# Kernel optimization log

Hardware: AMD Instinct MI355X
Metric: run time of the kernel (lower is better)

Reference implementation:

```python
import jax, jax.numpy as jnp
import numpy as np

INPUT_SIZE = 968
HIDDEN = 128
ESP = 1e-6


def _gru_scan(xp, w_hh, b_hh):
    # xp: [T, B, 3H] precomputed input projections; returns [T, B, H]
    B = xp.shape[1]
    h0 = jnp.zeros((B, HIDDEN), dtype=xp.dtype)

    def step(h, xp_t):
        gi_r, gi_z, gi_n = jnp.split(xp_t, 3, axis=-1)
        gh = h @ w_hh.T + b_hh
        gh_r, gh_z, gh_n = jnp.split(gh, 3, axis=-1)
        r = jax.nn.sigmoid(gi_r + gh_r)
        z = jax.nn.sigmoid(gi_z + gh_z)
        n = jnp.tanh(gi_n + r * gh_n)
        h_new = (1.0 - z) * n + z * h
        return h_new, h_new

    _, hs = jax.lax.scan(step, h0, xp)
    return hs


def _bigru_ln(x, w_ih_f, w_hh_f, b_ih_f, b_hh_f,
              w_ih_b, w_hh_b, b_ih_b, b_hh_b, ln_w, ln_b):
    # x: [B, T, D] (batch_first)
    # precompute input projections as one big GEMM per direction
    xp_f = jnp.einsum('btd,gd->btg', x, w_ih_f) + b_ih_f  # [B,T,3H]
    xp_b = jnp.einsum('btd,gd->btg', x, w_ih_b) + b_ih_b
    xp_f = jnp.swapaxes(xp_f, 0, 1)  # [T,B,3H]
    xp_b = jnp.swapaxes(xp_b, 0, 1)[::-1]  # reversed time for backward dir

    h_f = _gru_scan(xp_f, w_hh_f, b_hh_f)          # [T,B,H]
    h_b = _gru_scan(xp_b, w_hh_b, b_hh_b)[::-1]    # [T,B,H], un-reverse

    out = jnp.concatenate([h_f, h_b], axis=-1)     # [T,B,2H]
    out = jnp.swapaxes(out, 0, 1)                  # [B,T,2H]

    # LayerNormal: uses unbiased std (torch.std default, ddof=1), clamped
    mu = jnp.mean(out, axis=-1, keepdims=True)
    sigma = jnp.std(out, axis=-1, keepdims=True, ddof=1)
    sigma = jnp.maximum(sigma, ESP)
    return (out - mu) / sigma * ln_w + ln_b


def setup_inputs() -> dict:
    key = jax.random.key(0)
    ks = jax.random.split(key, 10)
    B, T = 64, 512
    s_ih = 1.0 / np.sqrt(HIDDEN)
    u = lambda k, shape: jax.random.uniform(k, shape, jnp.float32, -s_ih, s_ih)
    return {
        'x': jax.random.normal(ks[0], (B, T, INPUT_SIZE), jnp.float32),
        'w_ih_f': u(ks[1], (3 * HIDDEN, INPUT_SIZE)),
        'w_hh_f': u(ks[2], (3 * HIDDEN, HIDDEN)),
        'b_ih_f': u(ks[3], (3 * HIDDEN,)),
        'b_hh_f': u(ks[4], (3 * HIDDEN,)),
        'w_ih_b': u(ks[5], (3 * HIDDEN, INPUT_SIZE)),
        'w_hh_b': u(ks[6], (3 * HIDDEN, HIDDEN)),
        'b_ih_b': u(ks[7], (3 * HIDDEN,)),
        'b_hh_b': u(ks[8], (3 * HIDDEN,)),
        'ln_w': jnp.ones((2 * HIDDEN,), jnp.float32),
        'ln_b': jnp.zeros((2 * HIDDEN,), jnp.float32),
    }


def reference(x, w_ih_f, w_hh_f, b_ih_f, b_hh_f,
              w_ih_b, w_hh_b, b_ih_b, b_hh_b, ln_w, ln_b):
    return _bigru_ln(x, w_ih_f, w_hh_f, b_ih_f, b_hh_f,
                     w_ih_b, w_hh_b, b_ih_b, b_hh_b, ln_w, ln_b)
```

## Files before the change

### kernel.cpp

```cpp
#include <hip/hip_runtime.h>
#include <stdint.h>


#define LOG2E 1.4426950408889634f
#define TT 512
#define D_IN 968
#define KP 992
#define NOUT 768
#define HID 128

typedef __attribute__((ext_vector_type(8))) short short8;
typedef __attribute__((ext_vector_type(4))) float f32x4;
typedef __attribute__((ext_vector_type(4))) unsigned int u32x4;
typedef __attribute__((ext_vector_type(2))) unsigned int u32x2;

__device__ __forceinline__ unsigned short f2bf(float f) {
  unsigned u = __builtin_bit_cast(unsigned, f);
  u += 0x7FFFu + ((u >> 16) & 1u);
  return (unsigned short)(u >> 16);
}
__device__ __forceinline__ unsigned pack2bf(float a, float b) {
  return (unsigned)f2bf(a) | ((unsigned)f2bf(b) << 16);
}
__device__ __forceinline__ float exp2_(float x) { return __builtin_amdgcn_exp2f(x); }
__device__ __forceinline__ float rcp_(float x)  { return __builtin_amdgcn_rcpf(x); }

__device__ __forceinline__ void async_load16(const void* g, void* l) {
  __builtin_amdgcn_global_load_lds(
      (const __attribute__((address_space(1))) unsigned int*)g,
      (__attribute__((address_space(3))) unsigned int*)l, 16, 0, 0);
}

__device__ __forceinline__ void wg_barrier_lds() {
  asm volatile("s_waitcnt lgkmcnt(0)\n\ts_barrier" ::: "memory");
}

#define WIH_BYTES (NOUT * KP * 2)
#define WHH_BYTES (NOUT * HID * 2)
#define BIAS_BYTES 3072
#define BASE_OFF (WIH_BYTES + WHH_BYTES + BIAS_BYTES)
#define XBF_BYTES ((size_t)32768 * KP * 2)
#define XP_BYTES ((size_t)32768 * NOUT * 4)

__global__ __launch_bounds__(256) void kx_convert(const float* __restrict__ X,
                                                  unsigned short* __restrict__ Xb) {
  const long row = blockIdx.x;
  const int t = threadIdx.x;
  if (t < 242) {
    f32x4 v = *(const f32x4*)(X + row * D_IN + t * 4);
    u32x2 p = {pack2bf(v.x, v.y), pack2bf(v.z, v.w)};
    *(u32x2*)(Xb + row * KP + t * 4) = p;
  } else if (t < 248) {
    *(u32x2*)(Xb + row * KP + t * 4) = (u32x2){0, 0};
  }
}

__global__ __launch_bounds__(256) void k0_convert(
    const float* __restrict__ wihf, const float* __restrict__ whhf,
    const float* __restrict__ bihf, const float* __restrict__ wihb,
    const float* __restrict__ whhb, const float* __restrict__ bihb,
    unsigned short* __restrict__ wih16, unsigned short* __restrict__ whh16,
    float* __restrict__ bias_s) {
  int blk = blockIdx.x, tid = threadIdx.x;
  if (blk < NOUT) {
    int n = blk;
    float sc = ((n % 384) < 256) ? LOG2E : 2.0f * LOG2E;
    const float* src = (n < 384) ? (wihf + (long)n * D_IN) : (wihb + (long)(n - 384) * D_IN);
    for (int c = 0; c < 4; c++) {
      int k = c * 256 + tid;
      if (k < KP) {
        float v = (k < D_IN) ? src[k] * sc : 0.0f;
        wih16[(long)n * KP + k] = f2bf(v);
      }
    }
  } else if (blk < NOUT + 96) {
    int e0 = ((blk - NOUT) * 256 + tid) * 4;
    for (int i = 0; i < 4; i++) {
      int e = e0 + i;
      int m = e >> 7, k = e & 127;
      float sc = ((m % 384) < 256) ? LOG2E : 2.0f * LOG2E;
      float v = (m < 384) ? whhf[m * HID + k] : whhb[(m - 384) * HID + k];
      whh16[e] = f2bf(v * sc);
    }
  } else {
    for (int c = 0; c < 3; c++) {
      int n = c * 256 + tid;
      if (n < NOUT) {
        float sc = ((n % 384) < 256) ? LOG2E : 2.0f * LOG2E;
        bias_s[n] = ((n < 384) ? bihf[n] : bihb[n - 384]) * sc;
      }
    }
  }
}

__global__ __launch_bounds__(256, 2) void k1_gemm_fast(
    const unsigned short* __restrict__ Xb, const unsigned short* __restrict__ W,
    const float* __restrict__ bias_s, float* __restrict__ XP) {
  __shared__ unsigned short As[128 * 32];
  __shared__ unsigned short Bs[128 * 32];

  const int tid = threadIdx.x;
  const int lane = tid & 63, w = tid >> 6;
  const int q = lane >> 4, l15 = lane & 15;
  const int wr = w >> 1, wc = w & 1;
  const int nt = blockIdx.x;
  const int mt = blockIdx.y;
  const long R0 = (long)mt * 128;
  const int C0 = nt * 128;

  f32x4 acc[4][4];
#pragma unroll
  for (int i = 0; i < 4; i++)
#pragma unroll
    for (int j = 0; j < 4; j++) acc[i][j] = {0.f, 0.f, 0.f, 0.f};

  for (int it = 0; it < 31; it++) {
    const int k0 = it * 32;
#pragma unroll
    for (int c = 0; c < 2; c++) {
      int idx = c * 256 + w * 64 + lane;
      int row = idx >> 2, koff = (idx & 3) * 8;
      async_load16(Xb + (R0 + row) * KP + k0 + koff,
                   ((char*)As) + (c * 256 + w * 64) * 16);
      async_load16(W + (long)(C0 + row) * KP + k0 + koff,
                   ((char*)Bs) + (c * 256 + w * 64) * 16);
    }
    __syncthreads();
    short8 af[4], bf[4];
#pragma unroll
    for (int i = 0; i < 4; i++)
      af[i] = *(const short8*)&As[(wr * 64 + i * 16 + l15) * 32 + q * 8];
#pragma unroll
    for (int j = 0; j < 4; j++)
      bf[j] = *(const short8*)&Bs[(wc * 64 + j * 16 + l15) * 32 + q * 8];
#pragma unroll
    for (int i = 0; i < 4; i++)
#pragma unroll
      for (int j = 0; j < 4; j++)
        acc[i][j] = __builtin_amdgcn_mfma_f32_16x16x32_bf16(af[i], bf[j], acc[i][j], 0, 0, 0);
    __syncthreads();
  }
  float bv[4];
#pragma unroll
  for (int j = 0; j < 4; j++) bv[j] = bias_s[C0 + wc * 64 + j * 16 + l15];
#pragma unroll
  for (int i = 0; i < 4; i++)
#pragma unroll
    for (int j = 0; j < 4; j++) {
      int col = C0 + wc * 64 + j * 16 + l15;
      long Rb = R0 + wr * 64 + i * 16 + q * 4;
#pragma unroll
      for (int r = 0; r < 4; r++)
        XP[(Rb + r) * NOUT + col] = acc[i][j][r] + bv[j];
    }
}

#define AS_STRIDE 40
__global__ __launch_bounds__(256, 2) void k1_gemm_slow(
    const float* __restrict__ X, const unsigned short* __restrict__ W,
    const float* __restrict__ bias_s, float* __restrict__ XP) {
  __shared__ unsigned short As[128 * AS_STRIDE];
  __shared__ unsigned short Bs[128 * 32];
  const int tid = threadIdx.x;
  const int lane = tid & 63, w = tid >> 6;
  const int q = lane >> 4, l15 = lane & 15;
  const int wr = w >> 1, wc = w & 1;
  const int nt = blockIdx.x, mt = blockIdx.y;
  const long R0 = (long)mt * 128;
  const int C0 = nt * 128;
  const int ar = tid >> 1, ahf = tid & 1;
  f32x4 acc[4][4];
#pragma unroll
  for (int i = 0; i < 4; i++)
#pragma unroll
    for (int j = 0; j < 4; j++) acc[i][j] = {0.f, 0.f, 0.f, 0.f};
  const float* arow = X + (R0 + ar) * D_IN;
  for (int it = 0; it < 31; it++) {
    int k0 = it * 32;
    unsigned pk[8];
#pragma unroll
    for (int c = 0; c < 4; c++) {
      int kc = k0 + ahf * 16 + c * 4;
      kc = (kc <= 964) ? kc : 964;
      f32x4 v = *(const f32x4*)(arow + kc);
      pk[c * 2 + 0] = pack2bf(v.x, v.y);
      pk[c * 2 + 1] = pack2bf(v.z, v.w);
    }
    unsigned short* adst = &As[ar * AS_STRIDE + ahf * 16];
    *(u32x4*)adst = (u32x4){pk[0], pk[1], pk[2], pk[3]};
    *(u32x4*)(adst + 8) = (u32x4){pk[4], pk[5], pk[6], pk[7]};
#pragma unroll
    for (int c = 0; c < 2; c++) {
      int idx = c * 256 + w * 64 + lane;
      int brow = idx >> 2, koff = (idx & 3) * 8;
      async_load16(W + (long)(C0 + brow) * KP + k0 + koff,
                   ((char*)Bs) + (c * 256 + w * 64) * 16);
    }
    __syncthreads();
    short8 af[4], bf[4];
#pragma unroll
    for (int i = 0; i < 4; i++)
      af[i] = *(const short8*)&As[(wr * 64 + i * 16 + l15) * AS_STRIDE + q * 8];
#pragma unroll
    for (int j = 0; j < 4; j++)
      bf[j] = *(const short8*)&Bs[(wc * 64 + j * 16 + l15) * 32 + q * 8];
#pragma unroll
    for (int i = 0; i < 4; i++)
#pragma unroll
      for (int j = 0; j < 4; j++)
        acc[i][j] = __builtin_amdgcn_mfma_f32_16x16x32_bf16(af[i], bf[j], acc[i][j], 0, 0, 0);
    __syncthreads();
  }
  float bv[4];
#pragma unroll
  for (int j = 0; j < 4; j++) bv[j] = bias_s[C0 + wc * 64 + j * 16 + l15];
#pragma unroll
  for (int i = 0; i < 4; i++)
#pragma unroll
    for (int j = 0; j < 4; j++) {
      int col = C0 + wc * 64 + j * 16 + l15;
      long Rb = R0 + wr * 64 + i * 16 + q * 4;
#pragma unroll
      for (int r = 0; r < 4; r++)
        XP[(Rb + r) * NOUT + col] = acc[i][j][r] + bv[j];
    }
}

#define PF 4

__global__ __launch_bounds__(512) void k2_gru(
    const unsigned short* __restrict__ WHH, const float* __restrict__ XP,
    const float* __restrict__ bhh_f, const float* __restrict__ bhh_b,
    float* __restrict__ OUT) {
  __shared__ unsigned short Hl[2][16 * 128];

  const int tid = threadIdx.x;
  const int lane = tid & 63, w = tid >> 6;
  const int q = lane >> 4, b = lane & 15;
  const int dir = blockIdx.x & 1, bg = blockIdx.x >> 1;
  const int j0 = w * 16 + q * 4;

  for (int i = tid; i < 2 * 16 * 128; i += 512) ((unsigned short*)Hl)[i] = 0;

  short8 afr[3][4];
#pragma unroll
  for (int g = 0; g < 3; g++)
#pragma unroll
    for (int kt = 0; kt < 4; kt++) {
      int row = dir * 384 + g * 128 + w * 16 + b;
      afr[g][kt] = *(const short8*)(WHH + (long)row * HID + kt * 32 + q * 8);
    }
  const float* bhh = dir ? bhh_b : bhh_f;
  f32x4 bh[3];
#pragma unroll
  for (int g = 0; g < 3; g++) {
    f32x4 t = *(const f32x4*)(bhh + g * 128 + j0);
    bh[g] = t * ((g < 2) ? LOG2E : 2.0f * LOG2E);
  }

  const long gi_base = (long)(bg * 16 + b) * TT * NOUT + dir * 384 + j0;
  const long out_base = (long)(bg * 16 + b) * TT * 256 + dir * 128 + j0;

  f32x4 gR[PF], gZ[PF], gN[PF];
#pragma unroll
  for (int u = 0; u < PF; u++) {
    const int td = dir ? (TT - 1 - u) : u;
    const float* gb = XP + gi_base + (long)td * NOUT;
    gR[u] = *(const f32x4*)(gb);
    gZ[u] = *(const f32x4*)(gb + 128);
    gN[u] = *(const f32x4*)(gb + 256);
  }
  f32x4 h = {0.f, 0.f, 0.f, 0.f};
  __syncthreads();

  for (int t0 = 0; t0 < TT; t0 += PF) {
#pragma unroll
    for (int u = 0; u < PF; u++) {
      const int t = t0 + u;
      const int cur = t & 1, nxt = cur ^ 1;
      const int td = dir ? (TT - 1 - t) : t;

      short8 bfr[4];
#pragma unroll
      for (int kt = 0; kt < 4; kt++) {
        int ch = ((kt * 4 + q) ^ (b & 7)) * 8;
        bfr[kt] = *(const short8*)&Hl[cur][b * 128 + ch];
      }
      f32x4 accR = {0.f, 0.f, 0.f, 0.f};
      f32x4 accZ = {0.f, 0.f, 0.f, 0.f};
      f32x4 accN = {0.f, 0.f, 0.f, 0.f};
#pragma unroll
      for (int kt = 0; kt < 4; kt++) {
        accR = __builtin_amdgcn_mfma_f32_16x16x32_bf16(afr[0][kt], bfr[kt], accR, 0, 0, 0);
        accZ = __builtin_amdgcn_mfma_f32_16x16x32_bf16(afr[1][kt], bfr[kt], accZ, 0, 0, 0);
        accN = __builtin_amdgcn_mfma_f32_16x16x32_bf16(afr[2][kt], bfr[kt], accN, 0, 0, 0);
      }
      f32x4 hnew;
#pragma unroll
      for (int i = 0; i < 4; i++) {
        float pr = gR[u][i] + accR[i] + bh[0][i];
        float pz = gZ[u][i] + accZ[i] + bh[1][i];
        float r = rcp_(1.0f + exp2_(-pr));
        float z = rcp_(1.0f + exp2_(-pz));
        float pn = gN[u][i] + r * (accN[i] + bh[2][i]);
        float n = 1.0f - 2.0f * rcp_(exp2_(pn) + 1.0f);
        hnew[i] = n + z * (h[i] - n);
      }
      h = hnew;
      {
        int tn = t + PF;
        tn = (tn < TT) ? tn : (TT - 1);
        const int tdn = dir ? (TT - 1 - tn) : tn;
        const float* gb = XP + gi_base + (long)tdn * NOUT;
        gR[u] = *(const f32x4*)(gb);
        gZ[u] = *(const f32x4*)(gb + 128);
        gN[u] = *(const f32x4*)(gb + 256);
      }
      {
        int ch = ((j0 >> 3) ^ (b & 7)) * 8 + (j0 & 7);
        u32x2 hv = {pack2bf(hnew[0], hnew[1]), pack2bf(hnew[2], hnew[3])};
        *(u32x2*)&Hl[nxt][b * 128 + ch] = hv;
      }
      *(f32x4*)(OUT + out_base + (long)td * 256) = hnew;
      wg_barrier_lds();
    }
  }
}

__global__ __launch_bounds__(256) void k3_ln(float* __restrict__ OUT,
                                             const float* __restrict__ lnw,
                                             const float* __restrict__ lnb) {
  const int tid = threadIdx.x, lane = tid & 63, w = tid >> 6;
  const long row = (long)blockIdx.x * 4 + w;
  float* p = OUT + row * 256 + lane * 4;
  f32x4 x = *(const f32x4*)p;
  float s = x[0] + x[1] + x[2] + x[3];
  float s2 = x[0] * x[0] + x[1] * x[1] + x[2] * x[2] + x[3] * x[3];
#pragma unroll
  for (int m = 1; m < 64; m <<= 1) {
    s += __shfl_xor(s, m, 64);
    s2 += __shfl_xor(s2, m, 64);
  }
  float mu = s * (1.0f / 256.0f);
  float var = (s2 - s * mu) * (1.0f / 255.0f);
  var = fmaxf(var, 0.0f);
  float sig = fmaxf(sqrtf(var), 1e-6f);
  float inv = 1.0f / sig;
  f32x4 wv = *(const f32x4*)(lnw + lane * 4);
  f32x4 bv = *(const f32x4*)(lnb + lane * 4);
  f32x4 y;
#pragma unroll
  for (int i = 0; i < 4; i++) y[i] = (x[i] - mu) * inv * wv[i] + bv[i];
  *(f32x4*)p = y;
}

extern "C" void kernel_launch(void* const* d_in, const int* in_sizes, int n_in,
                              void* d_out, int out_size, void* d_ws, size_t ws_size,
                              hipStream_t stream) {
  const float* x = (const float*)d_in[0];
  const float* wihf = (const float*)d_in[1];
  const float* whhf = (const float*)d_in[2];
  const float* bihf = (const float*)d_in[3];
  const float* bhhf = (const float*)d_in[4];
  const float* wihb = (const float*)d_in[5];
  const float* whhb = (const float*)d_in[6];
  const float* bihb = (const float*)d_in[7];
  const float* bhhb = (const float*)d_in[8];
  const float* lnw = (const float*)d_in[9];
  const float* lnb = (const float*)d_in[10];

  char* ws = (char*)d_ws;
  unsigned short* wih16 = (unsigned short*)ws;
  unsigned short* whh16 = (unsigned short*)(ws + WIH_BYTES);
  float* bias_s = (float*)(ws + WIH_BYTES + WHH_BYTES);
  float* out = (float*)d_out;

  const size_t need_fast = (size_t)BASE_OFF + XBF_BYTES + XP_BYTES;

  hipLaunchKernelGGL(k0_convert, dim3(768 + 96 + 1), dim3(256), 0, stream,
                     wihf, whhf, bihf, wihb, whhb, bihb, wih16, whh16, bias_s);

  float* xp;
  if (ws_size >= need_fast) {
    unsigned short* xbf = (unsigned short*)(ws + BASE_OFF);
    xp = (float*)(ws + BASE_OFF + XBF_BYTES);
    hipLaunchKernelGGL(kx_convert, dim3(32768), dim3(256), 0, stream, x, xbf);
    hipLaunchKernelGGL(k1_gemm_fast, dim3(6, 256), dim3(256), 0, stream,
                       xbf, wih16, bias_s, xp);
  } else {
    xp = (float*)(ws + BASE_OFF);
    hipLaunchKernelGGL(k1_gemm_slow, dim3(6, 256), dim3(256), 0, stream,
                       x, wih16, bias_s, xp);
  }
  hipLaunchKernelGGL(k2_gru, dim3(8), dim3(512), 0, stream, whh16, xp, bhhf, bhhb, out);
  hipLaunchKernelGGL(k3_ln, dim3(8192), dim3(256), 0, stream, out, lnw, lnb);
}
```

Baseline: 683.2 us.

## Restructure GRU recurrence step: split MFMA chains, fold hidden biases, pointer-increment prefetch

Folds the r and z hidden-state biases into the precomputed input-projection bias so the recurrent step does fewer adds per element. The serial GRU step now splits each gate's 4-deep dependent MFMA chain into two independent 2-deep chains that are summed afterwards, shortening the critical latency per timestep. Address arithmetic is replaced by incremented pointers, and the tail iterations no longer issue redundant prefetch loads. The gate math is vectorized so the transcendental instructions can be grouped. The cost is a few extra vector adds per step and more registers held live.

Measured after the change: 703.3 us. 1.03x slower.

```diff
diff --git a/kernel.cpp b/kernel.cpp
--- a/kernel.cpp
+++ b/kernel.cpp
@@ -59,6 +59,7 @@
     const float* __restrict__ wihf, const float* __restrict__ whhf,
     const float* __restrict__ bihf, const float* __restrict__ wihb,
     const float* __restrict__ whhb, const float* __restrict__ bihb,
+    const float* __restrict__ bhhf, const float* __restrict__ bhhb,
     unsigned short* __restrict__ wih16, unsigned short* __restrict__ whh16,
     float* __restrict__ bias_s) {
   int blk = blockIdx.x, tid = threadIdx.x;
@@ -86,8 +87,12 @@
     for (int c = 0; c < 3; c++) {
       int n = c * 256 + tid;
       if (n < NOUT) {
-        float sc = ((n % 384) < 256) ? LOG2E : 2.0f * LOG2E;
-        bias_s[n] = ((n < 384) ? bihf[n] : bihb[n - 384]) * sc;
+        int g = (n % 384) >> 7;
+        float sc = (g < 2) ? LOG2E : 2.0f * LOG2E;
+        float bi = (n < 384) ? bihf[n] : bihb[n - 384];
+        float bh = (n < 384) ? bhhf[n] : bhhb[n - 384];
+        float v = (g < 2) ? (bi + bh) : bi;
+        bias_s[n] = v * sc;
       }
     }
   }
@@ -226,7 +231,72 @@
     }
 }
 
+__device__ __forceinline__ f32x4 gru_gate(f32x4 accR, f32x4 accZ, f32x4 accN,
+                                          f32x4 gr, f32x4 gz, f32x4 gn,
+                                          f32x4 bh2, f32x4 h) {
+  f32x4 pr = gr + accR;
+  f32x4 pz = gz + accZ;
+  f32x4 er, ez;
+#pragma unroll
+  for (int i = 0; i < 4; i++) er[i] = exp2_(-pr[i]);
+#pragma unroll
+  for (int i = 0; i < 4; i++) ez[i] = exp2_(-pz[i]);
+  f32x4 dr = er + 1.0f, dz = ez + 1.0f;
+  f32x4 r, z;
+#pragma unroll
+  for (int i = 0; i < 4; i++) r[i] = rcp_(dr[i]);
+#pragma unroll
+  for (int i = 0; i < 4; i++) z[i] = rcp_(dz[i]);
+  f32x4 pn = gn + r * (accN + bh2);
+  f32x4 en;
+#pragma unroll
+  for (int i = 0; i < 4; i++) en[i] = exp2_(pn[i]);
+  f32x4 dn = en + 1.0f, invn;
+#pragma unroll
+  for (int i = 0; i < 4; i++) invn[i] = rcp_(dn[i]);
+  f32x4 n = 1.0f - 2.0f * invn;
+  return n + z * (h - n);
+}
+
 #define PF 4
+#define MFMA_BF16 __builtin_amdgcn_mfma_f32_16x16x32_bf16
+
+#define K2_STEP(U, REFILL)                                                    \
+  {                                                                           \
+    const unsigned short* hb = ((U) & 1) ? hrd1 : hrd0;                       \
+    short8 b0 = *(const short8*)(hb + ch0);                                   \
+    short8 b1 = *(const short8*)(hb + ch1);                                   \
+    short8 b2 = *(const short8*)(hb + ch2);                                   \
+    short8 b3 = *(const short8*)(hb + ch3);                                   \
+    f32x4 cgR = gRr[U], cgZ = gZr[U], cgN = gNr[U];                           \
+    if (REFILL) {                                                             \
+      gRr[U] = *(const f32x4*)(gp);                                           \
+      gZr[U] = *(const f32x4*)(gp + 128);                                     \
+      gNr[U] = *(const f32x4*)(gp + 256);                                     \
+      gp += gstep;                                                            \
+    }                                                                         \
+    const f32x4 zz = {0.f, 0.f, 0.f, 0.f};                                    \
+    f32x4 aR0 = MFMA_BF16(afr[0][0], b0, zz, 0, 0, 0);                        \
+    f32x4 aZ0 = MFMA_BF16(afr[1][0], b0, zz, 0, 0, 0);                        \
+    f32x4 aN0 = MFMA_BF16(afr[2][0], b0, zz, 0, 0, 0);                        \
+    f32x4 aR1 = MFMA_BF16(afr[0][2], b2, zz, 0, 0, 0);                        \
+    f32x4 aZ1 = MFMA_BF16(afr[1][2], b2, zz, 0, 0, 0);                        \
+    f32x4 aN1 = MFMA_BF16(afr[2][2], b2, zz, 0, 0, 0);                        \
+    aR0 = MFMA_BF16(afr[0][1], b1, aR0, 0, 0, 0);                             \
+    aZ0 = MFMA_BF16(afr[1][1], b1, aZ0, 0, 0, 0);                             \
+    aN0 = MFMA_BF16(afr[2][1], b1, aN0, 0, 0, 0);                             \
+    aR1 = MFMA_BF16(afr[0][3], b3, aR1, 0, 0, 0);                             \
+    aZ1 = MFMA_BF16(afr[1][3], b3, aZ1, 0, 0, 0);                             \
+    aN1 = MFMA_BF16(afr[2][3], b3, aN1, 0, 0, 0);                             \
+    f32x4 hnew = gru_gate(aR0 + aR1, aZ0 + aZ1, aN0 + aN1,                    \
+                          cgR, cgZ, cgN, bh2, h);                             \
+    h = hnew;                                                                 \
+    u32x2 hv = {pack2bf(hnew[0], hnew[1]), pack2bf(hnew[2], hnew[3])};        \
+    *(u32x2*)(((U) & 1) ? hwr0 : hwr1) = hv;                                  \
+    *(f32x4*)op = hnew;                                                       \
+    op += ostep;                                                              \
+    wg_barrier_lds();                                                         \
+  }
 
 __global__ __launch_bounds__(512) void k2_gru(
     const unsigned short* __restrict__ WHH, const float* __restrict__ XP,
@@ -251,80 +321,46 @@
       afr[g][kt] = *(const short8*)(WHH + (long)row * HID + kt * 32 + q * 8);
     }
   const float* bhh = dir ? bhh_b : bhh_f;
-  f32x4 bh[3];
-#pragma unroll
-  for (int g = 0; g < 3; g++) {
-    f32x4 t = *(const f32x4*)(bhh + g * 128 + j0);
-    bh[g] = t * ((g < 2) ? LOG2E : 2.0f * LOG2E);
-  }
-
-  const long gi_base = (long)(bg * 16 + b) * TT * NOUT + dir * 384 + j0;
-  const long out_base = (long)(bg * 16 + b) * TT * 256 + dir * 128 + j0;
-
-  f32x4 gR[PF], gZ[PF], gN[PF];
+  f32x4 bh2 = (*(const f32x4*)(bhh + 256 + j0)) * (2.0f * LOG2E);
+
+  const long gstep = dir ? -(long)NOUT : (long)NOUT;
+  const long ostep = dir ? -256L : 256L;
+  const int td0 = dir ? (TT - 1) : 0;
+  const float* gp = XP + ((long)(bg * 16 + b) * TT + td0) * NOUT + dir * 384 + j0;
+  float* op = OUT + ((long)(bg * 16 + b) * TT + td0) * 256 + dir * 128 + j0;
+
+  f32x4 gRr[PF], gZr[PF], gNr[PF];
 #pragma unroll
   for (int u = 0; u < PF; u++) {
-    const int td = dir ? (TT - 1 - u) : u;
-    const float* gb = XP + gi_base + (long)td * NOUT;
-    gR[u] = *(const f32x4*)(gb);
-    gZ[u] = *(const f32x4*)(gb + 128);
-    gN[u] = *(const f32x4*)(gb + 256);
-  }
+    gRr[u] = *(const f32x4*)(gp);
+    gZr[u] = *(const f32x4*)(gp + 128);
+    gNr[u] = *(const f32x4*)(gp + 256);
+    gp += gstep;
+  }
+
+  const int ch0 = ((0 * 4 + q) ^ (b & 7)) * 8;
+  const int ch1 = ((1 * 4 + q) ^ (b & 7)) * 8;
+  const int ch2 = ((2 * 4 + q) ^ (b & 7)) * 8;
+  const int ch3 = ((3 * 4 + q) ^ (b & 7)) * 8;
+  const int chw = (((j0 >> 3) ^ (b & 7)) * 8) + (j0 & 7);
+  const unsigned short* hrd0 = &Hl[0][b * 128];
+  const unsigned short* hrd1 = &Hl[1][b * 128];
+  unsigned short* hwr0 = &Hl[0][b * 128 + chw];
+  unsigned short* hwr1 = &Hl[1][b * 128 + chw];
+
   f32x4 h = {0.f, 0.f, 0.f, 0.f};
   __syncthreads();
 
-  for (int t0 = 0; t0 < TT; t0 += PF) {
-#pragma unroll
-    for (int u = 0; u < PF; u++) {
-      const int t = t0 + u;
-      const int cur = t & 1, nxt = cur ^ 1;
-      const int td = dir ? (TT - 1 - t) : t;
-
-      short8 bfr[4];
-#pragma unroll
-      for (int kt = 0; kt < 4; kt++) {
-        int ch = ((kt * 4 + q) ^ (b & 7)) * 8;
-        bfr[kt] = *(const short8*)&Hl[cur][b * 128 + ch];
-      }
-      f32x4 accR = {0.f, 0.f, 0.f, 0.f};
-      f32x4 accZ = {0.f, 0.f, 0.f, 0.f};
-      f32x4 accN = {0.f, 0.f, 0.f, 0.f};
-#pragma unroll
-      for (int kt = 0; kt < 4; kt++) {
-        accR = __builtin_amdgcn_mfma_f32_16x16x32_bf16(afr[0][kt], bfr[kt], accR, 0, 0, 0);
-        accZ = __builtin_amdgcn_mfma_f32_16x16x32_bf16(afr[1][kt], bfr[kt], accZ, 0, 0, 0);
-        accN = __builtin_amdgcn_mfma_f32_16x16x32_bf16(afr[2][kt], bfr[kt], accN, 0, 0, 0);
-      }
-      f32x4 hnew;
-#pragma unroll
-      for (int i = 0; i < 4; i++) {
-        float pr = gR[u][i] + accR[i] + bh[0][i];
-        float pz = gZ[u][i] + accZ[i] + bh[1][i];
-        float r = rcp_(1.0f + exp2_(-pr));
-        float z = rcp_(1.0f + exp2_(-pz));
-        float pn = gN[u][i] + r * (accN[i] + bh[2][i]);
-        float n = 1.0f - 2.0f * rcp_(exp2_(pn) + 1.0f);
-        hnew[i] = n + z * (h[i] - n);
-      }
-      h = hnew;
-      {
-        int tn = t + PF;
-        tn = (tn < TT) ? tn : (TT - 1);
-        const int tdn = dir ? (TT - 1 - tn) : tn;
-        const float* gb = XP + gi_base + (long)tdn * NOUT;
-        gR[u] = *(const f32x4*)(gb);
-        gZ[u] = *(const f32x4*)(gb + 128);
-        gN[u] = *(const f32x4*)(gb + 256);
-      }
-      {
-        int ch = ((j0 >> 3) ^ (b & 7)) * 8 + (j0 & 7);
-        u32x2 hv = {pack2bf(hnew[0], hnew[1]), pack2bf(hnew[2], hnew[3])};
-        *(u32x2*)&Hl[nxt][b * 128 + ch] = hv;
-      }
-      *(f32x4*)(OUT + out_base + (long)td * 256) = hnew;
-      wg_barrier_lds();
-    }
-  }
+  for (int t0 = 0; t0 < TT - PF; t0 += PF) {
+    K2_STEP(0, 1)
+    K2_STEP(1, 1)
+    K2_STEP(2, 1)
+    K2_STEP(3, 1)
+  }
+  K2_STEP(0, 0)
+  K2_STEP(1, 0)
+  K2_STEP(2, 0)
+  K2_STEP(3, 0)
 }
 
 __global__ __launch_bounds__(256) void k3_ln(float* __restrict__ OUT,
@@ -378,7 +414,8 @@
   const size_t need_fast = (size_t)BASE_OFF + XBF_BYTES + XP_BYTES;
 
   hipLaunchKernelGGL(k0_convert, dim3(768 + 96 + 1), dim3(256), 0, stream,
-                     wihf, whhf, bihf, wihb, whhb, bihb, wih16, whh16, bias_s);
+                     wihf, whhf, bihf, wihb, whhb, bihb, bhhf, bhhb,
+                     wih16, whh16, bias_s);
 
   float* xp;
   if (ws_size >= need_fast) {
```
